# Kernel tuning notes

Hardware: AMD Instinct MI355X
Metric: run time of the kernel (lower is better)

## Reference

```python
import jax, jax.numpy as jnp
import numpy as np


def _gcn_conv(x, src, dst, num_nodes, W, b):
    """PyG GCNConv: add self-loops, symmetric normalization, scatter-add, bias."""
    h = x @ W  # [N, F_out]
    # degree over destination nodes (all edge weights are 1, incl. self-loops)
    deg = jax.ops.segment_sum(jnp.ones_like(dst, dtype=h.dtype), dst,
                              num_segments=num_nodes)
    deg_inv_sqrt = jnp.where(deg > 0, jax.lax.rsqrt(deg), 0.0)
    norm = deg_inv_sqrt[src] * deg_inv_sqrt[dst]  # [E+N]
    msg = h[src] * norm[:, None]                  # gather + scale
    out = jax.ops.segment_sum(msg, dst, num_segments=num_nodes)  # scatter-add
    return out + b


def setup_inputs() -> dict:
    key = jax.random.key(0)
    k_x, k_e, k_w1, k_w2 = jax.random.split(key, 4)
    N, E, F = 50000, 800000, 128
    x = jax.random.normal(k_x, (N, F), dtype=jnp.float32)
    edge_index = jax.random.randint(k_e, (2, E), 0, N, dtype=jnp.int64)
    scale = 1.0 / np.sqrt(F)
    W1 = jax.random.normal(k_w1, (F, F), dtype=jnp.float32) * scale
    b1 = jnp.zeros((F,), dtype=jnp.float32)
    W2 = jax.random.normal(k_w2, (F, F), dtype=jnp.float32) * scale
    b2 = jnp.zeros((F,), dtype=jnp.float32)
    return {"x": x, "edge_index": edge_index, "W1": W1, "b1": b1,
            "W2": W2, "b2": b2}


def reference(x, edge_index, W1, b1, W2, b2):
    num_nodes = x.shape[0]
    loops = jnp.arange(num_nodes, dtype=edge_index.dtype)
    src = jnp.concatenate([edge_index[0], loops])
    dst = jnp.concatenate([edge_index[1], loops])
    # layer 1: GCNConv -> Identity norm -> relu -> dropout(eval=identity)
    h = jax.nn.relu(_gcn_conv(x, src, dst, num_nodes, W1, b1))
    # layer 2 (last_activation=True, so relu again)
    out = jax.nn.relu(_gcn_conv(h, src, dst, num_nodes, W2, b2))
    return out
```

## Files before the change

### kernel.cpp

```cpp
#include <hip/hip_runtime.h>
#include <hip/hip_bf16.h>

#define CDIV(a,b) (((a)+(b)-1)/(b))

typedef __bf16 bf16x8 __attribute__((ext_vector_type(8)));
typedef float  f32x4  __attribute__((ext_vector_type(4)));

union Frag16 { uint4 u; bf16x8 f; unsigned short s[8]; };
union Pack8  { unsigned short s[4]; uint2 u; };

__device__ __forceinline__ unsigned short f2bf(float f) {
    unsigned u = __float_as_uint(f);
    return (unsigned short)((u + 0x7fff + ((u >> 16) & 1)) >> 16);
}
__device__ __forceinline__ float bf2f(unsigned short s) {
    return __uint_as_float(((unsigned)s) << 16);
}

__global__ void detect_kernel(const int* __restrict__ edges, int* __restrict__ flag, int E) {
    int n = min(E, 4096);
    int found = 0;
    for (int j = threadIdx.x; j < n; j += 256) found |= (edges[2 * j + 1] != 0);
    if (found) *flag = 1;
}

__device__ __forceinline__ int load_src(const int* e, int f, int E, int i) {
    return f ? e[i] : e[2 * i];
}
__device__ __forceinline__ int load_dst(const int* e, int f, int E, int i) {
    return f ? e[E + i] : e[2 * (E + i)];
}

__global__ void count_kernel(const int* __restrict__ edges, const int* __restrict__ flag,
                             int* __restrict__ counts_sh, int* __restrict__ rank,
                             int E, int N) {
    int e = blockIdx.x * blockDim.x + threadIdx.x;
    if (e >= E) return;
    int f = *flag;
    int d = load_dst(edges, f, E, e);
    int s = blockIdx.x & 7;
    int r = atomicAdd(&counts_sh[s * N + d], 1);
    rank[e] = (r << 3) | s;
}

__global__ void merge_kernel(int* __restrict__ counts_sh, int* __restrict__ counts, int N) {
    int d = blockIdx.x * blockDim.x + threadIdx.x;
    if (d >= N) return;
    int run = 0;
    #pragma unroll
    for (int s = 0; s < 8; ++s) {
        int v = counts_sh[s * N + d];
        counts_sh[s * N + d] = run;
        run += v;
    }
    counts[d] = run;
}

__global__ void dis_kernel(const int* __restrict__ counts, float* __restrict__ dis, int N) {
    int i = blockIdx.x * blockDim.x + threadIdx.x;
    if (i < N) dis[i] = rsqrtf((float)(counts[i] + 1));
}

__global__ __launch_bounds__(256) void scan1_kernel(const int* __restrict__ counts,
                                                    int* __restrict__ bsum, int N) {
    __shared__ int red[4];
    int tid = threadIdx.x;
    int base = blockIdx.x * 1024;
    int s = 0;
    #pragma unroll
    for (int j = 0; j < 4; ++j) {
        int idx = base + tid + j * 256;
        if (idx < N) s += counts[idx];
    }
    #pragma unroll
    for (int off = 32; off >= 1; off >>= 1) s += __shfl_down(s, off, 64);
    if ((tid & 63) == 0) red[tid >> 6] = s;
    __syncthreads();
    if (tid == 0) bsum[blockIdx.x] = red[0] + red[1] + red[2] + red[3];
}

__global__ void scan2_kernel(const int* __restrict__ bsum, int* __restrict__ boff,
                             int B, int* __restrict__ row_ptr, int N, int E) {
    int lane = threadIdx.x;
    int carry = 0;
    for (int base = 0; base < B; base += 64) {
        int i = base + lane;
        int v = (i < B) ? bsum[i] : 0;
        int x = v;
        #pragma unroll
        for (int off = 1; off < 64; off <<= 1) {
            int t = __shfl_up(x, off, 64);
            if (lane >= off) x += t;
        }
        if (i < B) boff[i] = carry + x - v;
        carry += __shfl(x, 63, 64);
    }
    if (lane == 0) row_ptr[N] = E;
}

__global__ __launch_bounds__(256) void scan3_kernel(const int* __restrict__ counts,
                                                    const int* __restrict__ boff,
                                                    int* __restrict__ row_ptr, int N) {
    __shared__ int wsum[4];
    int tid = threadIdx.x;
    int lane = tid & 63, wv = tid >> 6;
    int base = blockIdx.x * 1024 + tid * 4;
    int c[4];
    #pragma unroll
    for (int j = 0; j < 4; ++j) c[j] = (base + j < N) ? counts[base + j] : 0;
    int tsum = c[0] + c[1] + c[2] + c[3];
    int x = tsum;
    #pragma unroll
    for (int off = 1; off < 64; off <<= 1) {
        int t = __shfl_up(x, off, 64);
        if (lane >= off) x += t;
    }
    int texcl = x - tsum;
    if (lane == 63) wsum[wv] = x;
    __syncthreads();
    int woff = 0;
    for (int w = 0; w < wv; ++w) woff += wsum[w];
    int off0 = boff[blockIdx.x] + woff + texcl;
    int run = 0;
    #pragma unroll
    for (int j = 0; j < 4; ++j) {
        if (base + j < N) row_ptr[base + j] = off0 + run;
        run += c[j];
    }
}

__global__ void fill_kernel(const int* __restrict__ edges, const int* __restrict__ flag,
                            const int* __restrict__ row_ptr, const int* __restrict__ rank,
                            const int* __restrict__ counts_sh,
                            const float* __restrict__ dis, int2* __restrict__ edata,
                            int E, int N) {
    int e = blockIdx.x * blockDim.x + threadIdx.x;
    if (e >= E) return;
    int f = *flag;
    int s = load_src(edges, f, E, e);
    int d = load_dst(edges, f, E, e);
    int rk = rank[e];
    int sh = rk & 7;
    int pos = row_ptr[d] + counts_sh[sh * N + d] + (rk >> 3);
    edata[pos] = make_int2(s, __float_as_int(dis[s]));
}

__global__ __launch_bounds__(256) void wprep_kernel(const float* __restrict__ W,
                                                    unsigned short* __restrict__ Wfh,
                                                    unsigned short* __restrict__ Wfl) {
    __shared__ float Wld[128][128];
    int tid = threadIdx.x;
    #pragma unroll
    for (int it = 0; it < 16; ++it) {
        int f = it * 256 + tid;
        int r = f >> 5, c4 = f & 31;
        *(float4*)(&Wld[r][c4 * 4]) = *(const float4*)(W + r * 128 + c4 * 4);
    }
    __syncthreads();
    #pragma unroll
    for (int it = 0; it < 8; ++it) {
        int c = it * 256 + tid;
        int ntk = c >> 6;
        int lane = c & 63;
        int ks = ntk & 3;
        int ntile = ntk >> 2;
        int quad = lane >> 4, nlo = lane & 15;
        int n = ntile * 16 + nlo;
        Frag16 h, l;
        #pragma unroll
        for (int j = 0; j < 8; ++j) {
            float w = Wld[ks * 32 + quad * 8 + j][n];
            h.s[j] = f2bf(w);
            float rr = w - bf2f(h.s[j]);
            l.s[j] = f2bf(rr);
        }
        *(uint4*)(Wfh + (size_t)c * 8) = h.u;
        *(uint4*)(Wfl + (size_t)c * 8) = l.u;
    }
}

__global__ __launch_bounds__(256) void gemm_mfma_kernel(const float* __restrict__ X,
                                                        const unsigned short* __restrict__ Wfh,
                                                        const unsigned short* __restrict__ Wfl,
                                                        unsigned short* __restrict__ out16,
                                                        int N) {
    __shared__ unsigned short Xh[64][136];
    __shared__ unsigned short Xl[64][136];
    int tid = threadIdx.x;
    int row0 = blockIdx.x * 64;
    #pragma unroll
    for (int it = 0; it < 8; ++it) {
        int f = it * 256 + tid;
        int r = f >> 5, c4 = f & 31;
        float4 v = make_float4(0.f, 0.f, 0.f, 0.f);
        int gr = row0 + r;
        if (gr < N) v = *(const float4*)(X + (size_t)gr * 128 + c4 * 4);
        float vv[4] = {v.x, v.y, v.z, v.w};
        Pack8 h, l;
        #pragma unroll
        for (int j = 0; j < 4; ++j) {
            h.s[j] = f2bf(vv[j]);
            float rr = vv[j] - bf2f(h.s[j]);
            l.s[j] = f2bf(rr);
        }
        *(uint2*)(&Xh[r][c4 * 4]) = h.u;
        *(uint2*)(&Xl[r][c4 * 4]) = l.u;
    }
    __syncthreads();

    int lane = tid & 63;
    int wv = tid >> 6;
    int quad = lane >> 4, nlo = lane & 15;
    f32x4 acc[8];
    #pragma unroll
    for (int t = 0; t < 8; ++t) acc[t] = (f32x4){0.f, 0.f, 0.f, 0.f};

    #pragma unroll
    for (int ks = 0; ks < 4; ++ks) {
        int kcol = ks * 32 + quad * 8;
        Frag16 xh, xl;
        xh.u = *(const uint4*)(&Xh[wv * 16 + nlo][kcol]);
        xl.u = *(const uint4*)(&Xl[wv * 16 + nlo][kcol]);
        #pragma unroll
        for (int t = 0; t < 8; ++t) {
            size_t cidx = ((size_t)(t * 4 + ks) * 64 + lane) * 8;
            Frag16 wh, wl;
            wh.u = *(const uint4*)(Wfh + cidx);
            wl.u = *(const uint4*)(Wfl + cidx);
            acc[t] = __builtin_amdgcn_mfma_f32_16x16x32_bf16(xh.f, wh.f, acc[t], 0, 0, 0);
            acc[t] = __builtin_amdgcn_mfma_f32_16x16x32_bf16(xh.f, wl.f, acc[t], 0, 0, 0);
            acc[t] = __builtin_amdgcn_mfma_f32_16x16x32_bf16(xl.f, wh.f, acc[t], 0, 0, 0);
        }
    }
    #pragma unroll
    for (int rg = 0; rg < 4; ++rg) {
        int gr = row0 + wv * 16 + quad * 4 + rg;
        if (gr < N) {
            #pragma unroll
            for (int t = 0; t < 8; ++t)
                out16[(size_t)gr * 128 + t * 16 + nlo] = f2bf(acc[t][rg]);
        }
    }
}

__global__ __launch_bounds__(256) void agg_kernel(const unsigned short* __restrict__ H16,
                                                  const int* __restrict__ row_ptr,
                                                  const int2* __restrict__ edata,
                                                  const float* __restrict__ dis,
                                                  const float* __restrict__ bias,
                                                  float* __restrict__ out, int N) {
    int wid = (blockIdx.x * blockDim.x + threadIdx.x) >> 6;
    int lane = threadIdx.x & 63;
    if (wid >= N) return;
    const ushort2* H2 = (const ushort2*)H16;
    float dd = dis[wid];
    ushort2 hv = H2[(size_t)wid * 64 + lane];
    float wself = dd * dd;
    float2 acc = make_float2(bf2f(hv.x) * wself, bf2f(hv.y) * wself);
    int e0 = __builtin_amdgcn_readfirstlane(row_ptr[wid]);
    int e1 = __builtin_amdgcn_readfirstlane(row_ptr[wid + 1]);
    for (int e = e0; e < e1; e += 8) {
        int rem = e1 - e;
        int   sj[8];
        float wj[8];
        #pragma unroll
        for (int j = 0; j < 8; ++j) {
            bool valid = j < rem;
            int2 ed = edata[valid ? e + j : e];
            sj[j] = ed.x;
            wj[j] = valid ? __int_as_float(ed.y) * dd : 0.f;
        }
        ushort2 aj[8];
        #pragma unroll
        for (int j = 0; j < 8; ++j)
            aj[j] = H2[(size_t)sj[j] * 64 + lane];
        #pragma unroll
        for (int j = 0; j < 8; ++j) {
            acc.x += bf2f(aj[j].x) * wj[j];
            acc.y += bf2f(aj[j].y) * wj[j];
        }
    }
    float2 b = ((const float2*)bias)[lane];
    float2 o = make_float2(fmaxf(acc.x + b.x, 0.f), fmaxf(acc.y + b.y, 0.f));
    ((float2*)out)[(size_t)wid * 64 + lane] = o;
}

extern "C" void kernel_launch(void* const* d_in, const int* in_sizes, int n_in,
                              void* d_out, int out_size, void* d_ws, size_t ws_size,
                              hipStream_t stream) {
    const float* x    = (const float*)d_in[0];
    const int*  edges = (const int*)d_in[1];
    const float* W1   = (const float*)d_in[2];
    const float* b1   = (const float*)d_in[3];
    const float* W2   = (const float*)d_in[4];
    const float* b2   = (const float*)d_in[5];
    float* out = (float*)d_out;

    const int F = 128;
    const int N = in_sizes[0] / F;
    const int E = in_sizes[1] / 2;
    const int NB = CDIV(N, 1024);

    #define AL4(v) (((v) + 3) & ~3)
    unsigned short* A16 = (unsigned short*)d_ws;
    float* B        = (float*)(A16 + (size_t)AL4(N * F));
    float* dis      = B + (size_t)AL4(N * F);
    int*  counts    = (int*)(dis + AL4(N));
    int*  counts_sh = counts + AL4(N);
    int*  flag      = counts_sh + AL4(8 * N);
    int*  row_ptr   = flag + 4;
    int*  bsum      = row_ptr + AL4(N + 1);
    int*  boff      = bsum + 64;
    int*  rank      = boff + 64;
    int2* edata     = (int2*)(rank + AL4(E));
    unsigned short* Wf1h = (unsigned short*)(edata + E);
    unsigned short* Wf1l = Wf1h + 16384;
    unsigned short* Wf2h = Wf1l + 16384;
    unsigned short* Wf2l = Wf2h + 16384;

    size_t zero_ints = (size_t)AL4(N) + AL4(8 * N) + 4;
    hipMemsetAsync(counts, 0, zero_ints * sizeof(int), stream);

    detect_kernel<<<1, 256, 0, stream>>>(edges, flag, E);
    count_kernel<<<CDIV(E, 256), 256, 0, stream>>>(edges, flag, counts_sh, rank, E, N);
    merge_kernel<<<CDIV(N, 256), 256, 0, stream>>>(counts_sh, counts, N);
    dis_kernel<<<CDIV(N, 256), 256, 0, stream>>>(counts, dis, N);
    scan1_kernel<<<NB, 256, 0, stream>>>(counts, bsum, N);
    scan2_kernel<<<1, 64, 0, stream>>>(bsum, boff, NB, row_ptr, N, E);
    scan3_kernel<<<NB, 256, 0, stream>>>(counts, boff, row_ptr, N);
    fill_kernel<<<CDIV(E, 256), 256, 0, stream>>>(edges, flag, row_ptr, rank,
                                                  counts_sh, dis, edata, E, N);
    wprep_kernel<<<1, 256, 0, stream>>>(W1, Wf1h, Wf1l);
    wprep_kernel<<<1, 256, 0, stream>>>(W2, Wf2h, Wf2l);

    gemm_mfma_kernel<<<CDIV(N, 64), 256, 0, stream>>>(x, Wf1h, Wf1l, A16, N);
    agg_kernel<<<CDIV(N * 64, 256), 256, 0, stream>>>(A16, row_ptr, edata, dis, b1, B, N);
    gemm_mfma_kernel<<<CDIV(N, 64), 256, 0, stream>>>(B, Wf2h, Wf2l, A16, N);
    agg_kernel<<<CDIV(N * 64, 256), 256, 0, stream>>>(A16, row_ptr, edata, dis, b2, out, N);
}
```

Measured before the change: 248.5 us.

## Merge preprocessing kernels and co-schedule first GEMM with edge counting

Folds weight prep and edge-format detection into one three-block launch. Runs the first-layer GEMM and the per-edge degree counting in a single heterogeneous grid so the two independent phases overlap. Also fuses merge, degree-inverse-sqrt and block-sum scan into one kernel, cutting several small launches and shrinking the memset. The cost is that the fat kernel reserves GEMM shared memory for the counting blocks too, which can lower their occupancy.

Result: faster. 229.5 us (-7.6%).

```diff
diff --git a/kernel.cpp b/kernel.cpp
--- a/kernel.cpp
+++ b/kernel.cpp
@@ -17,13 +17,6 @@
     return __uint_as_float(((unsigned)s) << 16);
 }
 
-__global__ void detect_kernel(const int* __restrict__ edges, int* __restrict__ flag, int E) {
-    int n = min(E, 4096);
-    int found = 0;
-    for (int j = threadIdx.x; j < n; j += 256) found |= (edges[2 * j + 1] != 0);
-    if (found) *flag = 1;
-}
-
 __device__ __forceinline__ int load_src(const int* e, int f, int E, int i) {
     return f ? e[i] : e[2 * i];
 }
@@ -31,10 +24,127 @@
     return f ? e[E + i] : e[2 * (E + i)];
 }
 
-__global__ void count_kernel(const int* __restrict__ edges, const int* __restrict__ flag,
-                             int* __restrict__ counts_sh, int* __restrict__ rank,
-                             int E, int N) {
-    int e = blockIdx.x * blockDim.x + threadIdx.x;
+__global__ __launch_bounds__(256) void prep_kernel(const float* __restrict__ W1,
+                                                   const float* __restrict__ W2,
+                                                   unsigned short* __restrict__ Wf1h,
+                                                   unsigned short* __restrict__ Wf1l,
+                                                   unsigned short* __restrict__ Wf2h,
+                                                   unsigned short* __restrict__ Wf2l,
+                                                   const int* __restrict__ edges,
+                                                   int* __restrict__ flag, int E) {
+    int tid = threadIdx.x;
+    if (blockIdx.x == 2) {
+        int n = min(E, 4096);
+        int found = 0;
+        for (int j = tid; j < n; j += 256) found |= (edges[2 * j + 1] != 0);
+        if (found) *flag = 1;
+        return;
+    }
+    const float* W = (blockIdx.x == 0) ? W1 : W2;
+    unsigned short* Wfh = (blockIdx.x == 0) ? Wf1h : Wf2h;
+    unsigned short* Wfl = (blockIdx.x == 0) ? Wf1l : Wf2l;
+    #pragma unroll
+    for (int it = 0; it < 8; ++it) {
+        int c = it * 256 + tid;
+        int ntk = c >> 6;
+        int lane = c & 63;
+        int ks = ntk & 3;
+        int ntile = ntk >> 2;
+        int quad = lane >> 4, nlo = lane & 15;
+        int n = ntile * 16 + nlo;
+        Frag16 h, l;
+        #pragma unroll
+        for (int j = 0; j < 8; ++j) {
+            float w = W[(ks * 32 + quad * 8 + j) * 128 + n];
+            h.s[j] = f2bf(w);
+            float rr = w - bf2f(h.s[j]);
+            l.s[j] = f2bf(rr);
+        }
+        *(uint4*)(Wfh + (size_t)c * 8) = h.u;
+        *(uint4*)(Wfl + (size_t)c * 8) = l.u;
+    }
+}
+
+__device__ __forceinline__ void gemm_body(const float* __restrict__ X,
+                                          const unsigned short* __restrict__ Wfh,
+                                          const unsigned short* __restrict__ Wfl,
+                                          unsigned short* __restrict__ out16,
+                                          int N, int blk,
+                                          unsigned short (*Xh)[136],
+                                          unsigned short (*Xl)[136]) {
+    int tid = threadIdx.x;
+    int row0 = blk * 64;
+    #pragma unroll
+    for (int it = 0; it < 8; ++it) {
+        int f = it * 256 + tid;
+        int r = f >> 5, c4 = f & 31;
+        float4 v = make_float4(0.f, 0.f, 0.f, 0.f);
+        int gr = row0 + r;
+        if (gr < N) v = *(const float4*)(X + (size_t)gr * 128 + c4 * 4);
+        float vv[4] = {v.x, v.y, v.z, v.w};
+        Pack8 h, l;
+        #pragma unroll
+        for (int j = 0; j < 4; ++j) {
+            h.s[j] = f2bf(vv[j]);
+            float rr = vv[j] - bf2f(h.s[j]);
+            l.s[j] = f2bf(rr);
+        }
+        *(uint2*)(&Xh[r][c4 * 4]) = h.u;
+        *(uint2*)(&Xl[r][c4 * 4]) = l.u;
+    }
+    __syncthreads();
+
+    int lane = tid & 63;
+    int wv = tid >> 6;
+    int quad = lane >> 4, nlo = lane & 15;
+    f32x4 acc[8];
+    #pragma unroll
+    for (int t = 0; t < 8; ++t) acc[t] = (f32x4){0.f, 0.f, 0.f, 0.f};
+
+    #pragma unroll
+    for (int ks = 0; ks < 4; ++ks) {
+        int kcol = ks * 32 + quad * 8;
+        Frag16 xh, xl;
+        xh.u = *(const uint4*)(&Xh[wv * 16 + nlo][kcol]);
+        xl.u = *(const uint4*)(&Xl[wv * 16 + nlo][kcol]);
+        #pragma unroll
+        for (int t = 0; t < 8; ++t) {
+            size_t cidx = ((size_t)(t * 4 + ks) * 64 + lane) * 8;
+            Frag16 wh, wl;
+            wh.u = *(const uint4*)(Wfh + cidx);
+            wl.u = *(const uint4*)(Wfl + cidx);
+            acc[t] = __builtin_amdgcn_mfma_f32_16x16x32_bf16(xh.f, wh.f, acc[t], 0, 0, 0);
+            acc[t] = __builtin_amdgcn_mfma_f32_16x16x32_bf16(xh.f, wl.f, acc[t], 0, 0, 0);
+            acc[t] = __builtin_amdgcn_mfma_f32_16x16x32_bf16(xl.f, wh.f, acc[t], 0, 0, 0);
+        }
+    }
+    #pragma unroll
+    for (int rg = 0; rg < 4; ++rg) {
+        int gr = row0 + wv * 16 + quad * 4 + rg;
+        if (gr < N) {
+            #pragma unroll
+            for (int t = 0; t < 8; ++t)
+                out16[(size_t)gr * 128 + t * 16 + nlo] = f2bf(acc[t][rg]);
+        }
+    }
+}
+
+__global__ __launch_bounds__(256) void fat_kernel(const float* __restrict__ X,
+                                                  const unsigned short* __restrict__ Wfh,
+                                                  const unsigned short* __restrict__ Wfl,
+                                                  unsigned short* __restrict__ out16,
+                                                  int N, int Ggemm,
+                                                  const int* __restrict__ edges,
+                                                  const int* __restrict__ flag,
+                                                  int* __restrict__ counts_sh,
+                                                  int* __restrict__ rank, int E) {
+    __shared__ unsigned short Xh[64][136];
+    __shared__ unsigned short Xl[64][136];
+    if (blockIdx.x < (unsigned)Ggemm) {
+        gemm_body(X, Wfh, Wfl, out16, N, blockIdx.x, Xh, Xl);
+        return;
+    }
+    int e = (blockIdx.x - Ggemm) * 256 + threadIdx.x;
     if (e >= E) return;
     int f = *flag;
     int d = load_dst(edges, f, E, e);
@@ -43,38 +153,42 @@
     rank[e] = (r << 3) | s;
 }
 
-__global__ void merge_kernel(int* __restrict__ counts_sh, int* __restrict__ counts, int N) {
-    int d = blockIdx.x * blockDim.x + threadIdx.x;
-    if (d >= N) return;
-    int run = 0;
-    #pragma unroll
-    for (int s = 0; s < 8; ++s) {
-        int v = counts_sh[s * N + d];
-        counts_sh[s * N + d] = run;
-        run += v;
-    }
-    counts[d] = run;
-}
-
-__global__ void dis_kernel(const int* __restrict__ counts, float* __restrict__ dis, int N) {
-    int i = blockIdx.x * blockDim.x + threadIdx.x;
-    if (i < N) dis[i] = rsqrtf((float)(counts[i] + 1));
-}
-
-__global__ __launch_bounds__(256) void scan1_kernel(const int* __restrict__ counts,
-                                                    int* __restrict__ bsum, int N) {
+__global__ __launch_bounds__(256) void gemm_mfma_kernel(const float* __restrict__ X,
+                                                        const unsigned short* __restrict__ Wfh,
+                                                        const unsigned short* __restrict__ Wfl,
+                                                        unsigned short* __restrict__ out16,
+                                                        int N) {
+    __shared__ unsigned short Xh[64][136];
+    __shared__ unsigned short Xl[64][136];
+    gemm_body(X, Wfh, Wfl, out16, N, blockIdx.x, Xh, Xl);
+}
+
+__global__ __launch_bounds__(256) void merge_dis_kernel(int* __restrict__ counts_sh,
+                                                        int* __restrict__ counts,
+                                                        float* __restrict__ dis,
+                                                        int* __restrict__ bsum, int N) {
     __shared__ int red[4];
     int tid = threadIdx.x;
-    int base = blockIdx.x * 1024;
-    int s = 0;
+    int bs = 0;
     #pragma unroll
     for (int j = 0; j < 4; ++j) {
-        int idx = base + tid + j * 256;
-        if (idx < N) s += counts[idx];
-    }
-    #pragma unroll
-    for (int off = 32; off >= 1; off >>= 1) s += __shfl_down(s, off, 64);
-    if ((tid & 63) == 0) red[tid >> 6] = s;
+        int d = blockIdx.x * 1024 + j * 256 + tid;
+        if (d < N) {
+            int run = 0;
+            #pragma unroll
+            for (int s = 0; s < 8; ++s) {
+                int v = counts_sh[s * N + d];
+                counts_sh[s * N + d] = run;
+                run += v;
+            }
+            counts[d] = run;
+            dis[d] = rsqrtf((float)(run + 1));
+            bs += run;
+        }
+    }
+    #pragma unroll
+    for (int off = 32; off >= 1; off >>= 1) bs += __shfl_down(bs, off, 64);
+    if ((tid & 63) == 0) red[tid >> 6] = bs;
     __syncthreads();
     if (tid == 0) bsum[blockIdx.x] = red[0] + red[1] + red[2] + red[3];
 }
@@ -143,104 +257,6 @@
     int sh = rk & 7;
     int pos = row_ptr[d] + counts_sh[sh * N + d] + (rk >> 3);
     edata[pos] = make_int2(s, __float_as_int(dis[s]));
-}
-
-__global__ __launch_bounds__(256) void wprep_kernel(const float* __restrict__ W,
-                                                    unsigned short* __restrict__ Wfh,
-                                                    unsigned short* __restrict__ Wfl) {
-    __shared__ float Wld[128][128];
-    int tid = threadIdx.x;
-    #pragma unroll
-    for (int it = 0; it < 16; ++it) {
-        int f = it * 256 + tid;
-        int r = f >> 5, c4 = f & 31;
-        *(float4*)(&Wld[r][c4 * 4]) = *(const float4*)(W + r * 128 + c4 * 4);
-    }
-    __syncthreads();
-    #pragma unroll
-    for (int it = 0; it < 8; ++it) {
-        int c = it * 256 + tid;
-        int ntk = c >> 6;
-        int lane = c & 63;
-        int ks = ntk & 3;
-        int ntile = ntk >> 2;
-        int quad = lane >> 4, nlo = lane & 15;
-        int n = ntile * 16 + nlo;
-        Frag16 h, l;
-        #pragma unroll
-        for (int j = 0; j < 8; ++j) {
-            float w = Wld[ks * 32 + quad * 8 + j][n];
-            h.s[j] = f2bf(w);
-            float rr = w - bf2f(h.s[j]);
-            l.s[j] = f2bf(rr);
-        }
-        *(uint4*)(Wfh + (size_t)c * 8) = h.u;
-        *(uint4*)(Wfl + (size_t)c * 8) = l.u;
-    }
-}
-
-__global__ __launch_bounds__(256) void gemm_mfma_kernel(const float* __restrict__ X,
-                                                        const unsigned short* __restrict__ Wfh,
-                                                        const unsigned short* __restrict__ Wfl,
-                                                        unsigned short* __restrict__ out16,
-                                                        int N) {
-    __shared__ unsigned short Xh[64][136];
-    __shared__ unsigned short Xl[64][136];
-    int tid = threadIdx.x;
-    int row0 = blockIdx.x * 64;
-    #pragma unroll
-    for (int it = 0; it < 8; ++it) {
-        int f = it * 256 + tid;
-        int r = f >> 5, c4 = f & 31;
-        float4 v = make_float4(0.f, 0.f, 0.f, 0.f);
-        int gr = row0 + r;
-        if (gr < N) v = *(const float4*)(X + (size_t)gr * 128 + c4 * 4);
-        float vv[4] = {v.x, v.y, v.z, v.w};
-        Pack8 h, l;
-        #pragma unroll
-        for (int j = 0; j < 4; ++j) {
-            h.s[j] = f2bf(vv[j]);
-            float rr = vv[j] - bf2f(h.s[j]);
-            l.s[j] = f2bf(rr);
-        }
-        *(uint2*)(&Xh[r][c4 * 4]) = h.u;
-        *(uint2*)(&Xl[r][c4 * 4]) = l.u;
-    }
-    __syncthreads();
-
-    int lane = tid & 63;
-    int wv = tid >> 6;
-    int quad = lane >> 4, nlo = lane & 15;
-    f32x4 acc[8];
-    #pragma unroll
-    for (int t = 0; t < 8; ++t) acc[t] = (f32x4){0.f, 0.f, 0.f, 0.f};
-
-    #pragma unroll
-    for (int ks = 0; ks < 4; ++ks) {
-        int kcol = ks * 32 + quad * 8;
-        Frag16 xh, xl;
-        xh.u = *(const uint4*)(&Xh[wv * 16 + nlo][kcol]);
-        xl.u = *(const uint4*)(&Xl[wv * 16 + nlo][kcol]);
-        #pragma unroll
-        for (int t = 0; t < 8; ++t) {
-            size_t cidx = ((size_t)(t * 4 + ks) * 64 + lane) * 8;
-            Frag16 wh, wl;
-            wh.u = *(const uint4*)(Wfh + cidx);
-            wl.u = *(const uint4*)(Wfl + cidx);
-            acc[t] = __builtin_amdgcn_mfma_f32_16x16x32_bf16(xh.f, wh.f, acc[t], 0, 0, 0);
-            acc[t] = __builtin_amdgcn_mfma_f32_16x16x32_bf16(xh.f, wl.f, acc[t], 0, 0, 0);
-            acc[t] = __builtin_amdgcn_mfma_f32_16x16x32_bf16(xl.f, wh.f, acc[t], 0, 0, 0);
-        }
-    }
-    #pragma unroll
-    for (int rg = 0; rg < 4; ++rg) {
-        int gr = row0 + wv * 16 + quad * 4 + rg;
-        if (gr < N) {
-            #pragma unroll
-            for (int t = 0; t < 8; ++t)
-                out16[(size_t)gr * 128 + t * 16 + nlo] = f2bf(acc[t][rg]);
-        }
-    }
 }
 
 __global__ __launch_bounds__(256) void agg_kernel(const unsigned short* __restrict__ H16,
@@ -300,6 +316,8 @@
     const int N = in_sizes[0] / F;
     const int E = in_sizes[1] / 2;
     const int NB = CDIV(N, 1024);
+    const int Ggemm = CDIV(N, 64);
+    const int Gcount = CDIV(E, 256);
 
     #define AL4(v) (((v) + 3) & ~3)
     unsigned short* A16 = (unsigned short*)d_ws;
@@ -318,22 +336,17 @@
     unsigned short* Wf2h = Wf1l + 16384;
     unsigned short* Wf2l = Wf2h + 16384;
 
-    size_t zero_ints = (size_t)AL4(N) + AL4(8 * N) + 4;
-    hipMemsetAsync(counts, 0, zero_ints * sizeof(int), stream);
-
-    detect_kernel<<<1, 256, 0, stream>>>(edges, flag, E);
-    count_kernel<<<CDIV(E, 256), 256, 0, stream>>>(edges, flag, counts_sh, rank, E, N);
-    merge_kernel<<<CDIV(N, 256), 256, 0, stream>>>(counts_sh, counts, N);
-    dis_kernel<<<CDIV(N, 256), 256, 0, stream>>>(counts, dis, N);
-    scan1_kernel<<<NB, 256, 0, stream>>>(counts, bsum, N);
+    hipMemsetAsync(counts_sh, 0, ((size_t)AL4(8 * N) + 4) * sizeof(int), stream);
+
+    prep_kernel<<<3, 256, 0, stream>>>(W1, W2, Wf1h, Wf1l, Wf2h, Wf2l, edges, flag, E);
+    fat_kernel<<<Ggemm + Gcount, 256, 0, stream>>>(x, Wf1h, Wf1l, A16, N, Ggemm,
+                                                   edges, flag, counts_sh, rank, E);
+    merge_dis_kernel<<<NB, 256, 0, stream>>>(counts_sh, counts, dis, bsum, N);
     scan2_kernel<<<1, 64, 0, stream>>>(bsum, boff, NB, row_ptr, N, E);
     scan3_kernel<<<NB, 256, 0, stream>>>(counts, boff, row_ptr, N);
-    fill_kernel<<<CDIV(E, 256), 256, 0, stream>>>(edges, flag, row_ptr, rank,
-                                                  counts_sh, dis, edata, E, N);
-    wprep_kernel<<<1, 256, 0, stream>>>(W1, Wf1h, Wf1l);
-    wprep_kernel<<<1, 256, 0, stream>>>(W2, Wf2h, Wf2l);
-
-    gemm_mfma_kernel<<<CDIV(N, 64), 256, 0, stream>>>(x, Wf1h, Wf1l, A16, N);
+    fill_kernel<<<Gcount, 256, 0, stream>>>(edges, flag, row_ptr, rank,
+                                            counts_sh, dis, edata, E, N);
+
     agg_kernel<<<CDIV(N * 64, 256), 256, 0, stream>>>(A16, row_ptr, edata, dis, b1, B, N);
     gemm_mfma_kernel<<<CDIV(N, 64), 256, 0, stream>>>(B, Wf2h, Wf2l, A16, N);
     agg_kernel<<<CDIV(N * 64, 256), 256, 0, stream>>>(A16, row_ptr, edata, dis, b2, out, N);
```
